# Performance work log

Hardware: AMD Instinct MI355X
Metric: run time of the kernel (lower is better)

The kernel has to match this reference:

```python
import jax, jax.numpy as jnp
import numpy as np

NUM_HEADS = 16


def _local_attn(q, k, v, bias, nq, nk):
    """Blocked local attention, faithful to rearrange_to_dense_trunk semantics.
    q,k,v: [B,H,N,D]; bias: [B,Hb,N,N] (Hb broadcasts against H).
    Trunk i (queries [i*nq,(i+1)*nq)) attends keys at original indices
    [i*nq - pad_left, i*nq - pad_left + nk); out-of-range keys/values/bias are
    zero-padded (the module pads with zeros, no -inf key masking).
    Assumes N % nq == 0 (q_pad_length == 0, so the query mask loop is a no-op).
    """
    B, H, N, D = q.shape
    T = N // nq                      # n_trunks
    pad_left = (nk - nq) // 2
    Lp = (T - 1) * nq + nk           # padded key length so every window is full
    pad_right = Lp - pad_left - N
    k_p = jnp.pad(k, ((0, 0), (0, 0), (pad_left, pad_right), (0, 0)))
    v_p = jnp.pad(v, ((0, 0), (0, 0), (pad_left, pad_right), (0, 0)))
    b_p = jnp.pad(bias, ((0, 0), (0, 0), (0, 0), (pad_left, pad_right)))
    # window gather indices: [T, nk]
    kidx = jnp.arange(T)[:, None] * nq + jnp.arange(nk)[None, :]
    k_t = k_p[:, :, kidx, :]         # [B,H,T,nk,D]
    v_t = v_p[:, :, kidx, :]         # [B,H,T,nk,D]
    Bb, Hb = bias.shape[0], bias.shape[1]
    b_r = b_p.reshape(Bb, Hb, T, nq, Lp)
    b_t = jnp.take_along_axis(b_r, kidx[None, None, :, None, :], axis=-1)  # [Bb,Hb,T,nq,nk]
    q_t = q.reshape(B, H, T, nq, D)
    scores = jnp.einsum('bhtqd,bhtkd->bhtqk', q_t, k_t) + b_t
    w = jax.nn.softmax(scores, axis=-1)
    o = jnp.einsum('bhtqk,bhtkd->bhtqd', w, v_t)
    return o.reshape(B, H, N, D)


def setup_inputs() -> dict:
    key = jax.random.key(0)
    ks = jax.random.split(key, 8)
    B, N, C = 1, 4096, 256
    H, D = NUM_HEADS, 64
    HD = H * D
    q_x = jax.random.normal(ks[0], (B, N, C), dtype=jnp.float32)
    kv_x = jax.random.normal(ks[1], (B, N, C), dtype=jnp.float32)
    attn_bias = jax.random.normal(ks[2], (B, 1, N, N), dtype=jnp.float32) * 0.1
    Wq = jax.random.normal(ks[3], (C, HD), dtype=jnp.float32) / np.sqrt(C).astype(np.float32)
    Wk = jax.random.normal(ks[4], (C, HD), dtype=jnp.float32) / np.sqrt(C).astype(np.float32)
    Wv = jax.random.normal(ks[5], (C, HD), dtype=jnp.float32) / np.sqrt(C).astype(np.float32)
    Wg = jax.random.normal(ks[6], (C, HD), dtype=jnp.float32) / np.sqrt(C).astype(np.float32)
    Wo = jax.random.normal(ks[7], (HD, C), dtype=jnp.float32) / np.sqrt(HD).astype(np.float32)
    return {"q_x": q_x, "kv_x": kv_x, "attn_bias": attn_bias,
            "Wq": Wq, "Wk": Wk, "Wv": Wv, "Wg": Wg, "Wo": Wo,
            "n_queries": 64, "n_keys": 256}


def reference(q_x, kv_x, attn_bias, Wq, Wk, Wv, Wg, Wo, n_queries, n_keys):
    B, N, C = q_x.shape
    H = NUM_HEADS
    D = Wq.shape[-1] // H
    def split_heads(x):
        return x.reshape(B, N, H, D).transpose(0, 2, 1, 3)  # [B,H,N,D]
    q = split_heads(q_x @ Wq) / jnp.sqrt(jnp.float32(D))
    k = split_heads(kv_x @ Wk)
    v = split_heads(kv_x @ Wv)
    o = _local_attn(q, k, v, attn_bias, n_queries, n_keys)
    o = o.transpose(0, 2, 1, 3).reshape(B, N, H * D)
    g = jax.nn.sigmoid(q_x @ Wg)  # gating head
    return (o * g) @ Wo
```

## Files before the change

### kernel.cpp

```cpp
#include <hip/hip_runtime.h>

#define N_ 4096
#define C_ 256
#define H_ 16
#define D_ 64
#define HD_ 1024

typedef __attribute__((ext_vector_type(8))) __bf16 bf16x8;
typedef __attribute__((ext_vector_type(4))) __bf16 bf16x4;
typedef __attribute__((ext_vector_type(8))) _Float16 f16x8;
typedef __attribute__((ext_vector_type(4))) _Float16 f16x4;
typedef __attribute__((ext_vector_type(4))) float f32x4;

__device__ __forceinline__ void gload16(const void* g, void* l) {
    __builtin_amdgcn_global_load_lds(
        (const __attribute__((address_space(1))) unsigned int*)g,
        (__attribute__((address_space(3))) unsigned int*)l, 16, 0, 0);
}

struct bf2 { __bf16 h, l; };
__device__ __forceinline__ bf2 split_bf16(float v) {
    bf2 r;
    r.h = (__bf16)v;
    r.l = (__bf16)(v - (float)r.h);
    return r;
}

__global__ __launch_bounds__(256) void convert_kernel(
    const float* __restrict__ q_x, const float* __restrict__ kv_x,
    const float* __restrict__ Wq, const float* __restrict__ Wk,
    const float* __restrict__ Wv, const float* __restrict__ Wg,
    const float* __restrict__ Wo,
    _Float16* __restrict__ Xf, _Float16* __restrict__ WTf,
    __bf16* __restrict__ WoTh, __bf16* __restrict__ WoTl)
{
    __shared__ float ts[64][65];
    const int b = blockIdx.x;
    const int tid = threadIdx.x;

    if (b < 512) {
        const int seg = b >> 8;
        const float* src = seg ? kv_x : q_x;
        _Float16* df = Xf + (size_t)seg * 1048576;
        const int base = (b & 255) * 4096 + tid * 16;
#pragma unroll
        for (int q = 0; q < 4; ++q) {
            float4 v = *(const float4*)&src[base + q * 4];
            f16x4 fv;
            fv[0] = (_Float16)v.x; fv[1] = (_Float16)v.y;
            fv[2] = (_Float16)v.z; fv[3] = (_Float16)v.w;
            *(f16x4*)&df[base + q * 4] = fv;
        }
        return;
    }

    if (b < 768) {
        const int widx = (b - 512) >> 6;
        const int tile = (b - 512) & 63;
        const float* src = (widx == 0) ? Wq : (widx == 1) ? Wk : (widx == 2) ? Wv : Wg;
        _Float16* df = WTf + (size_t)widx * 262144;
        const int r0 = (tile >> 4) * 64;
        const int c0 = (tile & 15) * 64;
        {
            const int r = tid >> 2;
            const int cch = (tid & 3) * 16;
#pragma unroll
            for (int q = 0; q < 4; ++q) {
                float4 v = *(const float4*)&src[(size_t)(r0 + r) * 1024 + c0 + cch + q * 4];
                ts[r][cch + q * 4 + 0] = v.x;
                ts[r][cch + q * 4 + 1] = v.y;
                ts[r][cch + q * 4 + 2] = v.z;
                ts[r][cch + q * 4 + 3] = v.w;
            }
        }
        __syncthreads();
        {
            const int c = tid >> 2;
            const int rch = (tid & 3) * 16;
#pragma unroll
            for (int q = 0; q < 4; ++q) {
                f16x4 fv;
#pragma unroll
                for (int j = 0; j < 4; ++j)
                    fv[j] = (_Float16)ts[rch + q * 4 + j][c];
                *(f16x4*)&df[(size_t)(c0 + c) * 256 + r0 + rch + q * 4] = fv;
            }
        }
        return;
    }

    {
        const int tile = b - 768;
        const int r0 = (tile >> 2) * 64;
        const int c0 = (tile & 3) * 64;
        {
            const int r = tid >> 2;
            const int cch = (tid & 3) * 16;
#pragma unroll
            for (int q = 0; q < 4; ++q) {
                float4 v = *(const float4*)&Wo[(size_t)(r0 + r) * 256 + c0 + cch + q * 4];
                ts[r][cch + q * 4 + 0] = v.x;
                ts[r][cch + q * 4 + 1] = v.y;
                ts[r][cch + q * 4 + 2] = v.z;
                ts[r][cch + q * 4 + 3] = v.w;
            }
        }
        __syncthreads();
        {
            const int c = tid >> 2;
            const int rch = (tid & 3) * 16;
#pragma unroll
            for (int q = 0; q < 4; ++q) {
                bf16x4 hv, lv;
#pragma unroll
                for (int j = 0; j < 4; ++j) {
                    bf2 s = split_bf16(ts[rch + q * 4 + j][c]);
                    hv[j] = s.h; lv[j] = s.l;
                }
                *(bf16x4*)&WoTh[(size_t)(c0 + c) * 1024 + r0 + rch + q * 4] = hv;
                *(bf16x4*)&WoTl[(size_t)(c0 + c) * 1024 + r0 + rch + q * 4] = lv;
            }
        }
    }
}

__global__ __launch_bounds__(256) void proj_mfma(
    const _Float16* __restrict__ Xf, const _Float16* __restrict__ WTf,
    _Float16* __restrict__ qh, _Float16* __restrict__ kh,
    _Float16* __restrict__ vh, _Float16* __restrict__ gh)
{
    __shared__ __align__(16) char psmem[34816];
    _Float16* As = (_Float16*)psmem;
    _Float16* Bs = (_Float16*)(psmem + 16384);

    const int lb  = blockIdx.x;
    const int xcd = lb & 7;
    const int gr  = (lb >> 6) * 8 + xcd;
    const int g   = gr >> 5;
    const int m0  = (gr & 31) * 128;
    const int c0  = ((lb >> 3) & 7) * 128;

    const _Float16* A = Xf + ((g == 1 || g == 2) ? 1048576 : 0);
    const _Float16* B = WTf + (size_t)g * 262144;

    const int tid  = threadIdx.x;
    const int wave = tid >> 6;
    const int lane = tid & 63;
    const int wr   = wave >> 1;
    const int wc   = wave & 1;
    const int frow = lane & 15;
    const int grp  = lane >> 4;

    f32x4 acc[4][4];
#pragma unroll
    for (int i = 0; i < 4; ++i)
#pragma unroll
        for (int j = 0; j < 4; ++j) acc[i][j] = (f32x4){0.f, 0.f, 0.f, 0.f};

    const int srow = tid >> 3;
    const int sch  = tid & 7;

    for (int kt = 0; kt < 256; kt += 64) {
        __syncthreads();
#pragma unroll
        for (int p = 0; p < 4; ++p) {
            const int row = p * 32 + srow;
            const int koff = kt + ((sch ^ (row & 7)) << 3);
            gload16(A + (size_t)(m0 + row) * 256 + koff, (char*)As + p * 4096 + tid * 16);
            gload16(B + (size_t)(c0 + row) * 256 + koff, (char*)Bs + p * 4096 + tid * 16);
        }
        __syncthreads();

#pragma unroll
        for (int ks = 0; ks < 2; ++ks) {
            f16x8 af[4], bf[4];
#pragma unroll
            for (int f = 0; f < 4; ++f) {
                const int ra = wr * 64 + f * 16 + frow;
                const int rb = wc * 64 + f * 16 + frow;
                af[f] = *(const f16x8*)((char*)As + ra * 128 + (((ks * 4 + grp) ^ (ra & 7)) << 4));
                bf[f] = *(const f16x8*)((char*)Bs + rb * 128 + (((ks * 4 + grp) ^ (rb & 7)) << 4));
            }
#pragma unroll
            for (int i = 0; i < 4; ++i)
#pragma unroll
                for (int j = 0; j < 4; ++j)
                    acc[i][j] = __builtin_amdgcn_mfma_f32_16x16x32_f16(af[i], bf[j], acc[i][j], 0, 0, 0);
        }
    }

    __syncthreads();
    _Float16* Epi = (_Float16*)psmem;
    {
        const float scale = (g == 0) ? 0.125f : 1.f;
#pragma unroll
        for (int i = 0; i < 4; ++i)
#pragma unroll
            for (int j = 0; j < 4; ++j) {
                const int rr = wr * 64 + i * 16 + grp * 4;
                const int cc = wc * 64 + j * 16 + frow;
#pragma unroll
                for (int v = 0; v < 4; ++v) {
                    float x = acc[i][j][v];
                    x = (g == 3) ? 1.f / (1.f + __expf(-x)) : x * scale;
                    Epi[(rr + v) * 136 + cc] = (_Float16)x;
                }
            }
    }
    __syncthreads();
    {
        const int ch   = tid & 15;
        const int head = ch >> 3;
        const int e8   = (ch & 7) * 8;
#pragma unroll
        for (int p = 0; p < 8; ++p) {
            const int r = p * 16 + (tid >> 4);
            const f16x8 val = *(const f16x8*)&Epi[r * 136 + head * 64 + e8];
            if (g == 3) {
                *(f16x8*)&gh[(size_t)(m0 + r) * HD_ + c0 + head * 64 + e8] = val;
            } else {
                _Float16* dst = (g == 0) ? qh : (g == 1) ? kh : vh;
                const int hh = (c0 >> 6) + head;
                *(f16x8*)&dst[((size_t)hh * N_ + m0 + r) * D_ + e8] = val;
            }
        }
    }
}

__global__ __launch_bounds__(256) void attn_mfma(
    const _Float16* __restrict__ qh, const _Float16* __restrict__ kh,
    const _Float16* __restrict__ vh, const float* __restrict__ bias,
    const _Float16* __restrict__ gh,
    __bf16* __restrict__ o_hi, __bf16* __restrict__ o_lo)
{
    __shared__ __align__(16) char smem[59392];
    _Float16* Qs = (_Float16*)smem;
    char* Ks = smem + 8192;
    _Float16* Vs = (_Float16*)(smem + 8192);
    _Float16* Ps = (_Float16*)(smem + 25600);
    float* Oe = (float*)(smem + 25600);

    const int lb  = blockIdx.x;
    const int xcd = lb & 7;
    const int j_  = lb >> 3;
    const int h   = j_ >> 3;
    const int t   = xcd * 8 + (j_ & 7);
    const int tid = threadIdx.x;
    const int lane = tid & 63;
    const int wv = tid >> 6;
    const int frow = lane & 15;
    const int grp = lane >> 4;
    const int kbase = t * 64 - 96;

    const char* qbase = (const char*)qh + (size_t)(h * N_ + t * 64) * 128;
    const char* kbase_p = (const char*)kh + (size_t)h * N_ * 128;

#pragma unroll
    for (int q = 0; q < 2; ++q) {
        const int lin = q * 4096 + tid * 16;
        const int row = lin >> 7;
        const int ch = (lin >> 4) & 7;
        gload16(qbase + row * 128 + ((ch ^ (row & 7)) << 4), (char*)Qs + lin);
    }

    f32x4 sacc[16];

#pragma unroll
    for (int p = 0; p < 2; ++p) {
#pragma unroll
        for (int q = 0; q < 4; ++q) {
            const int lin = q * 4096 + tid * 16;
            const int row = lin >> 7;
            const int ch = (lin >> 4) & 7;
            const int kg = kbase + p * 128 + row;
            if ((unsigned)kg < (unsigned)N_) {
                gload16(kbase_p + (size_t)kg * 128 + ((ch ^ (row & 7)) << 4), Ks + lin);
            } else {
                *(float4*)(Ks + lin) = make_float4(0.f, 0.f, 0.f, 0.f);
            }
        }
        {
            const int rowg = t * 64 + wv * 16 + grp * 4;
#pragma unroll
            for (int j = 0; j < 8; ++j) {
                const int colg = kbase + p * 128 + j * 16 + frow;
                const bool ok = (unsigned)colg < (unsigned)N_;
#pragma unroll
                for (int v = 0; v < 4; ++v)
                    sacc[p * 8 + j][v] = ok ? bias[(size_t)(rowg + v) * N_ + colg] : 0.f;
            }
        }
        __syncthreads();
        const int rq = wv * 16 + frow;
#pragma unroll
        for (int ks = 0; ks < 2; ++ks) {
            const f16x8 aq = *(const f16x8*)((char*)Qs + rq * 128 + (((ks * 4 + grp) ^ (rq & 7)) << 4));
#pragma unroll
            for (int j = 0; j < 8; ++j) {
                const int rk = j * 16 + frow;
                const f16x8 bk = *(const f16x8*)(Ks + rk * 128 + (((ks * 4 + grp) ^ (rk & 7)) << 4));
                sacc[p * 8 + j] = __builtin_amdgcn_mfma_f32_16x16x32_f16(aq, bk, sacc[p * 8 + j], 0, 0, 0);
            }
        }
        __syncthreads();
    }

    float inv[4];
#pragma unroll
    for (int v = 0; v < 4; ++v) {
        float m = sacc[0][v];
#pragma unroll
        for (int f = 1; f < 16; ++f) m = fmaxf(m, sacc[f][v]);
        m = fmaxf(m, __shfl_xor(m, 1));
        m = fmaxf(m, __shfl_xor(m, 2));
        m = fmaxf(m, __shfl_xor(m, 4));
        m = fmaxf(m, __shfl_xor(m, 8));
        float l = 0.f;
#pragma unroll
        for (int f = 0; f < 16; ++f) {
            float e = __expf(sacc[f][v] - m);
            sacc[f][v] = e;
            l += e;
        }
        l += __shfl_xor(l, 1);
        l += __shfl_xor(l, 2);
        l += __shfl_xor(l, 4);
        l += __shfl_xor(l, 8);
        inv[v] = 1.f / l;
    }

    {
        const int rb = wv * 16 + grp * 4;
#pragma unroll
        for (int f = 0; f < 16; ++f) {
            const int col = (f >> 3) * 128 + (f & 7) * 16 + frow;
#pragma unroll
            for (int v = 0; v < 4; ++v)
                Ps[(rb + v) * 264 + col] = (_Float16)sacc[f][v];
        }
    }

    f32x4 oacc[4];
#pragma unroll
    for (int jd = 0; jd < 4; ++jd) oacc[jd] = (f32x4){0.f, 0.f, 0.f, 0.f};

#pragma unroll
    for (int c = 0; c < 2; ++c) {
        {
            const int sl = tid >> 1;
            const int d0 = (tid & 1) * 32;
            const int kg = kbase + c * 128 + sl;
            f16x8 vv[4];
            if ((unsigned)kg < (unsigned)N_) {
                const f16x8* vp = (const f16x8*)(vh + ((size_t)h * N_ + kg) * D_ + d0);
#pragma unroll
                for (int q = 0; q < 4; ++q) vv[q] = vp[q];
            } else {
#pragma unroll
                for (int q = 0; q < 4; ++q)
#pragma unroll
                    for (int e = 0; e < 8; ++e) vv[q][e] = (_Float16)0.f;
            }
#pragma unroll
            for (int q = 0; q < 4; ++q)
#pragma unroll
                for (int e = 0; e < 8; ++e)
                    Vs[(d0 + q * 8 + e) * 136 + sl] = vv[q][e];
        }
        __syncthreads();
        const int rp = wv * 16 + frow;
#pragma unroll
        for (int ks = 0; ks < 4; ++ks) {
            const f16x8 ap = *(const f16x8*)((char*)Ps + rp * 528 + c * 256 + ks * 64 + grp * 16);
#pragma unroll
            for (int jd = 0; jd < 4; ++jd) {
                const f16x8 bv = *(const f16x8*)((char*)Vs + (jd * 16 + frow) * 272 + ks * 64 + grp * 16);
                oacc[jd] = __builtin_amdgcn_mfma_f32_16x16x32_f16(ap, bv, oacc[jd], 0, 0, 0);
            }
        }
        __syncthreads();
    }

#pragma unroll
    for (int jd = 0; jd < 4; ++jd) {
        const int dcol = jd * 16 + frow;
#pragma unroll
        for (int v = 0; v < 4; ++v) {
            const int rn = wv * 16 + grp * 4 + v;
            Oe[rn * 68 + dcol] = oacc[jd][v] * inv[v];
        }
    }
    __syncthreads();
    {
        const int r   = tid >> 2;
        const int seg = tid & 3;
        const int n   = t * 64 + r;
        const int cg0 = h * 64 + seg * 16;
        const float* orow = &Oe[r * 68 + seg * 16];
        f32x4 o0 = *(const f32x4*)&orow[0];
        f32x4 o1 = *(const f32x4*)&orow[4];
        f32x4 o2 = *(const f32x4*)&orow[8];
        f32x4 o3 = *(const f32x4*)&orow[12];
        const f16x8 g0 = *(const f16x8*)&gh[(size_t)n * HD_ + cg0];
        const f16x8 g1 = *(const f16x8*)&gh[(size_t)n * HD_ + cg0 + 8];
        float vals[16];
#pragma unroll
        for (int e = 0; e < 4; ++e) {
            vals[e]      = o0[e] * (float)g0[e];
            vals[4 + e]  = o1[e] * (float)g0[4 + e];
            vals[8 + e]  = o2[e] * (float)g1[e];
            vals[12 + e] = o3[e] * (float)g1[4 + e];
        }
        bf16x8 hi0, hi1, lo0, lo1;
#pragma unroll
        for (int e = 0; e < 8; ++e) {
            bf2 s0 = split_bf16(vals[e]);
            bf2 s1 = split_bf16(vals[8 + e]);
            hi0[e] = s0.h; lo0[e] = s0.l;
            hi1[e] = s1.h; lo1[e] = s1.l;
        }
        *(bf16x8*)&o_hi[(size_t)n * HD_ + cg0]     = hi0;
        *(bf16x8*)&o_hi[(size_t)n * HD_ + cg0 + 8] = hi1;
        *(bf16x8*)&o_lo[(size_t)n * HD_ + cg0]     = lo0;
        *(bf16x8*)&o_lo[(size_t)n * HD_ + cg0 + 8] = lo1;
    }
}

__global__ __launch_bounds__(256) void out_mfma(
    const __bf16* __restrict__ o_hi, const __bf16* __restrict__ o_lo,
    const __bf16* __restrict__ WoTh, const __bf16* __restrict__ WoTl,
    float* __restrict__ out)
{
    __shared__ __align__(16) __bf16 smem[4 * 4096];
    __bf16* As_h = smem;
    __bf16* As_l = smem + 4096;
    __bf16* Bs_h = smem + 8192;
    __bf16* Bs_l = smem + 12288;

    const int lb  = blockIdx.x;
    const int xcd = lb & 7;
    const int idx = lb >> 3;
    const int rowg = (idx >> 2) * 8 + xcd;
    const int m0  = rowg * 64;
    const int c0  = (idx & 3) * 64;

    const int tid  = threadIdx.x;
    const int wave = tid >> 6;
    const int lane = tid & 63;
    const int wr   = wave >> 1;
    const int wc   = wave & 1;
    const int frow = lane & 15;
    const int grp  = lane >> 4;

    f32x4 acc[2][2];
#pragma unroll
    for (int i = 0; i < 2; ++i)
#pragma unroll
        for (int j = 0; j < 2; ++j) acc[i][j] = (f32x4){0.f, 0.f, 0.f, 0.f};

    for (int kt = 0; kt < 1024; kt += 64) {
        __syncthreads();
#pragma unroll
        for (int p = 0; p < 2; ++p) {
            const int lin = p * 4096 + tid * 16;
            const int row = lin >> 7;
            const int ch  = (lin >> 4) & 7;
            const int koff = kt + ((ch ^ (row & 7)) << 3);
            gload16(o_hi + (size_t)(m0 + row) * HD_ + koff, (char*)As_h + lin);
            gload16(o_lo + (size_t)(m0 + row) * HD_ + koff, (char*)As_l + lin);
            gload16(WoTh + (size_t)(c0 + row) * HD_ + koff, (char*)Bs_h + lin);
            gload16(WoTl + (size_t)(c0 + row) * HD_ + koff, (char*)Bs_l + lin);
        }
        __syncthreads();

#pragma unroll
        for (int ks = 0; ks < 2; ++ks) {
            bf16x8 afh[2], afl[2], bfh[2], bfl[2];
#pragma unroll
            for (int f = 0; f < 2; ++f) {
                const int ra = wr * 32 + f * 16 + frow;
                const int rb = wc * 32 + f * 16 + frow;
                const int ca = ((ks * 4 + grp) ^ (ra & 7)) << 4;
                const int cb = ((ks * 4 + grp) ^ (rb & 7)) << 4;
                afh[f] = *(const bf16x8*)((char*)As_h + ra * 128 + ca);
                afl[f] = *(const bf16x8*)((char*)As_l + ra * 128 + ca);
                bfh[f] = *(const bf16x8*)((char*)Bs_h + rb * 128 + cb);
                bfl[f] = *(const bf16x8*)((char*)Bs_l + rb * 128 + cb);
            }
#pragma unroll
            for (int i = 0; i < 2; ++i)
#pragma unroll
                for (int j = 0; j < 2; ++j) {
                    acc[i][j] = __builtin_amdgcn_mfma_f32_16x16x32_bf16(afh[i], bfh[j], acc[i][j], 0, 0, 0);
                    acc[i][j] = __builtin_amdgcn_mfma_f32_16x16x32_bf16(afl[i], bfh[j], acc[i][j], 0, 0, 0);
                    acc[i][j] = __builtin_amdgcn_mfma_f32_16x16x32_bf16(afh[i], bfl[j], acc[i][j], 0, 0, 0);
                }
        }
    }

    const int rbase = grp * 4;
#pragma unroll
    for (int i = 0; i < 2; ++i)
#pragma unroll
        for (int j = 0; j < 2; ++j) {
            const int c = c0 + wc * 32 + j * 16 + frow;
#pragma unroll
            for (int v = 0; v < 4; ++v) {
                const int n = m0 + wr * 32 + i * 16 + rbase + v;
                out[(size_t)n * C_ + c] = acc[i][j][v];
            }
        }
}

extern "C" void kernel_launch(void* const* d_in, const int* in_sizes, int n_in,
                              void* d_out, int out_size, void* d_ws, size_t ws_size,
                              hipStream_t stream)
{
    const float* q_x  = (const float*)d_in[0];
    const float* kv_x = (const float*)d_in[1];
    const float* bias = (const float*)d_in[2];
    const float* Wq   = (const float*)d_in[3];
    const float* Wk   = (const float*)d_in[4];
    const float* Wv   = (const float*)d_in[5];
    const float* Wg   = (const float*)d_in[6];
    const float* Wo   = (const float*)d_in[7];
    float* out = (float*)d_out;

    char* ws = (char*)d_ws;
    const size_t MB = 1048576;
    _Float16* qh  = (_Float16*)(ws);
    _Float16* kh  = (_Float16*)(ws + 8  * MB);
    _Float16* vh  = (_Float16*)(ws + 16 * MB);
    _Float16* gh  = (_Float16*)(ws + 24 * MB);
    __bf16* o_hi  = (__bf16*)(ws + 32 * MB);
    __bf16* o_lo  = (__bf16*)(ws + 40 * MB);
    _Float16* Xf  = (_Float16*)(ws + 48 * MB);
    _Float16* WTf = (_Float16*)(ws + 52 * MB);
    __bf16* WoTh  = (__bf16*)(ws + 54 * MB);
    __bf16* WoTl  = (__bf16*)(ws + 54 * MB + 524288);

    convert_kernel<<<832, 256, 0, stream>>>(q_x, kv_x, Wq, Wk, Wv, Wg, Wo,
                                            Xf, WTf, WoTh, WoTl);
    proj_mfma<<<1024, 256, 0, stream>>>(Xf, WTf, qh, kh, vh, gh);
    attn_mfma<<<1024, 256, 0, stream>>>(qh, kh, vh, bias, gh, o_hi, o_lo);
    out_mfma<<<256, 256, 0, stream>>>(o_hi, o_lo, WoTh, WoTl, out);
}
```

Measured before the change: 173.4 us.

## Use single fp16 output projection and shrink attention LDS footprint

Replaces the split-bf16 (hi/lo, 3-MFMA) output projection with a single fp16 operand path, so the attention output and Wo are each stored once in fp16 and out_mfma issues one MFMA per tile. The attention kernel now writes the P tile per key chunk into a smaller buffer that aliases Q/K space, cutting LDS from 59KB to 34KB, and adds a launch bound hint of 4 blocks per CU to raise occupancy. Together these reduce memory traffic, MFMA count and LDS pressure. The cost is lower precision in the final GEMM, since the fp16 rounding of gated outputs and weights replaces the near-fp32 split emulation, plus possible register pressure from the occupancy hint.

```diff
diff --git a/kernel.cpp b/kernel.cpp
--- a/kernel.cpp
+++ b/kernel.cpp
@@ -7,7 +7,6 @@
 #define HD_ 1024
 
 typedef __attribute__((ext_vector_type(8))) __bf16 bf16x8;
-typedef __attribute__((ext_vector_type(4))) __bf16 bf16x4;
 typedef __attribute__((ext_vector_type(8))) _Float16 f16x8;
 typedef __attribute__((ext_vector_type(4))) _Float16 f16x4;
 typedef __attribute__((ext_vector_type(4))) float f32x4;
@@ -16,14 +15,6 @@
     __builtin_amdgcn_global_load_lds(
         (const __attribute__((address_space(1))) unsigned int*)g,
         (__attribute__((address_space(3))) unsigned int*)l, 16, 0, 0);
-}
-
-struct bf2 { __bf16 h, l; };
-__device__ __forceinline__ bf2 split_bf16(float v) {
-    bf2 r;
-    r.h = (__bf16)v;
-    r.l = (__bf16)(v - (float)r.h);
-    return r;
 }
 
 __global__ __launch_bounds__(256) void convert_kernel(
@@ -32,7 +23,7 @@
     const float* __restrict__ Wv, const float* __restrict__ Wg,
     const float* __restrict__ Wo,
     _Float16* __restrict__ Xf, _Float16* __restrict__ WTf,
-    __bf16* __restrict__ WoTh, __bf16* __restrict__ WoTl)
+    _Float16* __restrict__ WoTf)
 {
     __shared__ float ts[64][65];
     const int b = blockIdx.x;
@@ -54,72 +45,47 @@
         return;
     }
 
+    const float* src;
+    _Float16* df;
+    int srcC, dstC, r0, c0;
     if (b < 768) {
         const int widx = (b - 512) >> 6;
         const int tile = (b - 512) & 63;
-        const float* src = (widx == 0) ? Wq : (widx == 1) ? Wk : (widx == 2) ? Wv : Wg;
-        _Float16* df = WTf + (size_t)widx * 262144;
-        const int r0 = (tile >> 4) * 64;
-        const int c0 = (tile & 15) * 64;
-        {
-            const int r = tid >> 2;
-            const int cch = (tid & 3) * 16;
-#pragma unroll
-            for (int q = 0; q < 4; ++q) {
-                float4 v = *(const float4*)&src[(size_t)(r0 + r) * 1024 + c0 + cch + q * 4];
-                ts[r][cch + q * 4 + 0] = v.x;
-                ts[r][cch + q * 4 + 1] = v.y;
-                ts[r][cch + q * 4 + 2] = v.z;
-                ts[r][cch + q * 4 + 3] = v.w;
-            }
-        }
-        __syncthreads();
-        {
-            const int c = tid >> 2;
-            const int rch = (tid & 3) * 16;
-#pragma unroll
-            for (int q = 0; q < 4; ++q) {
-                f16x4 fv;
-#pragma unroll
-                for (int j = 0; j < 4; ++j)
-                    fv[j] = (_Float16)ts[rch + q * 4 + j][c];
-                *(f16x4*)&df[(size_t)(c0 + c) * 256 + r0 + rch + q * 4] = fv;
-            }
-        }
-        return;
-    }
-
+        src = (widx == 0) ? Wq : (widx == 1) ? Wk : (widx == 2) ? Wv : Wg;
+        df = WTf + (size_t)widx * 262144;
+        srcC = 1024; dstC = 256;
+        r0 = (tile >> 4) * 64;
+        c0 = (tile & 15) * 64;
+    } else {
+        const int tile = b - 768;
+        src = Wo; df = WoTf;
+        srcC = 256; dstC = 1024;
+        r0 = (tile >> 2) * 64;
+        c0 = (tile & 3) * 64;
+    }
     {
-        const int tile = b - 768;
-        const int r0 = (tile >> 2) * 64;
-        const int c0 = (tile & 3) * 64;
-        {
-            const int r = tid >> 2;
-            const int cch = (tid & 3) * 16;
-#pragma unroll
-            for (int q = 0; q < 4; ++q) {
-                float4 v = *(const float4*)&Wo[(size_t)(r0 + r) * 256 + c0 + cch + q * 4];
-                ts[r][cch + q * 4 + 0] = v.x;
-                ts[r][cch + q * 4 + 1] = v.y;
-                ts[r][cch + q * 4 + 2] = v.z;
-                ts[r][cch + q * 4 + 3] = v.w;
-            }
-        }
-        __syncthreads();
-        {
-            const int c = tid >> 2;
-            const int rch = (tid & 3) * 16;
-#pragma unroll
-            for (int q = 0; q < 4; ++q) {
-                bf16x4 hv, lv;
-#pragma unroll
-                for (int j = 0; j < 4; ++j) {
-                    bf2 s = split_bf16(ts[rch + q * 4 + j][c]);
-                    hv[j] = s.h; lv[j] = s.l;
-                }
-                *(bf16x4*)&WoTh[(size_t)(c0 + c) * 1024 + r0 + rch + q * 4] = hv;
-                *(bf16x4*)&WoTl[(size_t)(c0 + c) * 1024 + r0 + rch + q * 4] = lv;
-            }
+        const int r = tid >> 2;
+        const int cch = (tid & 3) * 16;
+#pragma unroll
+        for (int q = 0; q < 4; ++q) {
+            float4 v = *(const float4*)&src[(size_t)(r0 + r) * srcC + c0 + cch + q * 4];
+            ts[r][cch + q * 4 + 0] = v.x;
+            ts[r][cch + q * 4 + 1] = v.y;
+            ts[r][cch + q * 4 + 2] = v.z;
+            ts[r][cch + q * 4 + 3] = v.w;
+        }
+    }
+    __syncthreads();
+    {
+        const int c = tid >> 2;
+        const int rch = (tid & 3) * 16;
+#pragma unroll
+        for (int q = 0; q < 4; ++q) {
+            f16x4 fv;
+#pragma unroll
+            for (int j = 0; j < 4; ++j)
+                fv[j] = (_Float16)ts[rch + q * 4 + j][c];
+            *(f16x4*)&df[(size_t)(c0 + c) * dstC + r0 + rch + q * 4] = fv;
         }
     }
 }
@@ -227,18 +193,17 @@
     }
 }
 
-__global__ __launch_bounds__(256) void attn_mfma(
+__global__ __launch_bounds__(256, 4) void attn_mfma(
     const _Float16* __restrict__ qh, const _Float16* __restrict__ kh,
     const _Float16* __restrict__ vh, const float* __restrict__ bias,
-    const _Float16* __restrict__ gh,
-    __bf16* __restrict__ o_hi, __bf16* __restrict__ o_lo)
+    const _Float16* __restrict__ gh, _Float16* __restrict__ of)
 {
-    __shared__ __align__(16) char smem[59392];
+    __shared__ __align__(16) char smem[34816];
     _Float16* Qs = (_Float16*)smem;
     char* Ks = smem + 8192;
-    _Float16* Vs = (_Float16*)(smem + 8192);
-    _Float16* Ps = (_Float16*)(smem + 25600);
-    float* Oe = (float*)(smem + 25600);
+    _Float16* Ps = (_Float16*)smem;
+    _Float16* Vs = (_Float16*)(smem + 17408);
+    float* Oe = (float*)smem;
 
     const int lb  = blockIdx.x;
     const int xcd = lb & 7;
@@ -329,17 +294,6 @@
         inv[v] = 1.f / l;
     }
 
-    {
-        const int rb = wv * 16 + grp * 4;
-#pragma unroll
-        for (int f = 0; f < 16; ++f) {
-            const int col = (f >> 3) * 128 + (f & 7) * 16 + frow;
-#pragma unroll
-            for (int v = 0; v < 4; ++v)
-                Ps[(rb + v) * 264 + col] = (_Float16)sacc[f][v];
-        }
-    }
-
     f32x4 oacc[4];
 #pragma unroll
     for (int jd = 0; jd < 4; ++jd) oacc[jd] = (f32x4){0.f, 0.f, 0.f, 0.f};
@@ -367,11 +321,21 @@
                 for (int e = 0; e < 8; ++e)
                     Vs[(d0 + q * 8 + e) * 136 + sl] = vv[q][e];
         }
+        {
+            const int rb = wv * 16 + grp * 4;
+#pragma unroll
+            for (int j = 0; j < 8; ++j) {
+                const int col = j * 16 + frow;
+#pragma unroll
+                for (int v = 0; v < 4; ++v)
+                    Ps[(rb + v) * 136 + col] = (_Float16)sacc[c * 8 + j][v];
+            }
+        }
         __syncthreads();
         const int rp = wv * 16 + frow;
 #pragma unroll
         for (int ks = 0; ks < 4; ++ks) {
-            const f16x8 ap = *(const f16x8*)((char*)Ps + rp * 528 + c * 256 + ks * 64 + grp * 16);
+            const f16x8 ap = *(const f16x8*)((char*)Ps + rp * 272 + ks * 64 + grp * 16);
 #pragma unroll
             for (int jd = 0; jd < 4; ++jd) {
                 const f16x8 bv = *(const f16x8*)((char*)Vs + (jd * 16 + frow) * 272 + ks * 64 + grp * 16);
@@ -403,39 +367,26 @@
         f32x4 o3 = *(const f32x4*)&orow[12];
         const f16x8 g0 = *(const f16x8*)&gh[(size_t)n * HD_ + cg0];
         const f16x8 g1 = *(const f16x8*)&gh[(size_t)n * HD_ + cg0 + 8];
-        float vals[16];
+        f16x8 r0, r1;
 #pragma unroll
         for (int e = 0; e < 4; ++e) {
-            vals[e]      = o0[e] * (float)g0[e];
-            vals[4 + e]  = o1[e] * (float)g0[4 + e];
-            vals[8 + e]  = o2[e] * (float)g1[e];
-            vals[12 + e] = o3[e] * (float)g1[4 + e];
-        }
-        bf16x8 hi0, hi1, lo0, lo1;
-#pragma unroll
-        for (int e = 0; e < 8; ++e) {
-            bf2 s0 = split_bf16(vals[e]);
-            bf2 s1 = split_bf16(vals[8 + e]);
-            hi0[e] = s0.h; lo0[e] = s0.l;
-            hi1[e] = s1.h; lo1[e] = s1.l;
-        }
-        *(bf16x8*)&o_hi[(size_t)n * HD_ + cg0]     = hi0;
-        *(bf16x8*)&o_hi[(size_t)n * HD_ + cg0 + 8] = hi1;
-        *(bf16x8*)&o_lo[(size_t)n * HD_ + cg0]     = lo0;
-        *(bf16x8*)&o_lo[(size_t)n * HD_ + cg0 + 8] = lo1;
+            r0[e]     = (_Float16)(o0[e] * (float)g0[e]);
+            r0[4 + e] = (_Float16)(o1[e] * (float)g0[4 + e]);
+            r1[e]     = (_Float16)(o2[e] * (float)g1[e]);
+            r1[4 + e] = (_Float16)(o3[e] * (float)g1[4 + e]);
+        }
+        *(f16x8*)&of[(size_t)n * HD_ + cg0]     = r0;
+        *(f16x8*)&of[(size_t)n * HD_ + cg0 + 8] = r1;
     }
 }
 
 __global__ __launch_bounds__(256) void out_mfma(
-    const __bf16* __restrict__ o_hi, const __bf16* __restrict__ o_lo,
-    const __bf16* __restrict__ WoTh, const __bf16* __restrict__ WoTl,
+    const _Float16* __restrict__ of, const _Float16* __restrict__ WoTf,
     float* __restrict__ out)
 {
-    __shared__ __align__(16) __bf16 smem[4 * 4096];
-    __bf16* As_h = smem;
-    __bf16* As_l = smem + 4096;
-    __bf16* Bs_h = smem + 8192;
-    __bf16* Bs_l = smem + 12288;
+    __shared__ __align__(16) _Float16 smem[2 * 4096];
+    _Float16* As = smem;
+    _Float16* Bs = smem + 4096;
 
     const int lb  = blockIdx.x;
     const int xcd = lb & 7;
@@ -466,35 +417,26 @@
             const int row = lin >> 7;
             const int ch  = (lin >> 4) & 7;
             const int koff = kt + ((ch ^ (row & 7)) << 3);
-            gload16(o_hi + (size_t)(m0 + row) * HD_ + koff, (char*)As_h + lin);
-            gload16(o_lo + (size_t)(m0 + row) * HD_ + koff, (char*)As_l + lin);
-            gload16(WoTh + (size_t)(c0 + row) * HD_ + koff, (char*)Bs_h + lin);
-            gload16(WoTl + (size_t)(c0 + row) * HD_ + koff, (char*)Bs_l + lin);
+            gload16(of   + (size_t)(m0 + row) * HD_ + koff, (char*)As + lin);
+            gload16(WoTf + (size_t)(c0 + row) * HD_ + koff, (char*)Bs + lin);
         }
         __syncthreads();
 
 #pragma unroll
         for (int ks = 0; ks < 2; ++ks) {
-            bf16x8 afh[2], afl[2], bfh[2], bfl[2];
+            f16x8 af[2], bf[2];
 #pragma unroll
             for (int f = 0; f < 2; ++f) {
                 const int ra = wr * 32 + f * 16 + frow;
                 const int rb = wc * 32 + f * 16 + frow;
-                const int ca = ((ks * 4 + grp) ^ (ra & 7)) << 4;
-                const int cb = ((ks * 4 + grp) ^ (rb & 7)) << 4;
-                afh[f] = *(const bf16x8*)((char*)As_h + ra * 128 + ca);
-                afl[f] = *(const bf16x8*)((char*)As_l + ra * 128 + ca);
-                bfh[f] = *(const bf16x8*)((char*)Bs_h + rb * 128 + cb);
-                bfl[f] = *(const bf16x8*)((char*)Bs_l + rb * 128 + cb);
+                af[f] = *(const f16x8*)((char*)As + ra * 128 + (((ks * 4 + grp) ^ (ra & 7)) << 4));
+                bf[f] = *(const f16x8*)((char*)Bs + rb * 128 + (((ks * 4 + grp) ^ (rb & 7)) << 4));
             }
 #pragma unroll
             for (int i = 0; i < 2; ++i)
 #pragma unroll
-                for (int j = 0; j < 2; ++j) {
-                    acc[i][j] = __builtin_amdgcn_mfma_f32_16x16x32_bf16(afh[i], bfh[j], acc[i][j], 0, 0, 0);
-                    acc[i][j] = __builtin_amdgcn_mfma_f32_16x16x32_bf16(afl[i], bfh[j], acc[i][j], 0, 0, 0);
-                    acc[i][j] = __builtin_amdgcn_mfma_f32_16x16x32_bf16(afh[i], bfl[j], acc[i][j], 0, 0, 0);
-                }
+                for (int j = 0; j < 2; ++j)
+                    acc[i][j] = __builtin_amdgcn_mfma_f32_16x16x32_f16(af[i], bf[j], acc[i][j], 0, 0, 0);
         }
     }
 
@@ -528,20 +470,18 @@
 
     char* ws = (char*)d_ws;
     const size_t MB = 1048576;
-    _Float16* qh  = (_Float16*)(ws);
-    _Float16* kh  = (_Float16*)(ws + 8  * MB);
-    _Float16* vh  = (_Float16*)(ws + 16 * MB);
-    _Float16* gh  = (_Float16*)(ws + 24 * MB);
-    __bf16* o_hi  = (__bf16*)(ws + 32 * MB);
-    __bf16* o_lo  = (__bf16*)(ws + 40 * MB);
-    _Float16* Xf  = (_Float16*)(ws + 48 * MB);
-    _Float16* WTf = (_Float16*)(ws + 52 * MB);
-    __bf16* WoTh  = (__bf16*)(ws + 54 * MB);
-    __bf16* WoTl  = (__bf16*)(ws + 54 * MB + 524288);
+    _Float16* qh   = (_Float16*)(ws);
+    _Float16* kh   = (_Float16*)(ws + 8  * MB);
+    _Float16* vh   = (_Float16*)(ws + 16 * MB);
+    _Float16* gh   = (_Float16*)(ws + 24 * MB);
+    _Float16* of   = (_Float16*)(ws + 32 * MB);
+    _Float16* Xf   = (_Float16*)(ws + 40 * MB);
+    _Float16* WTf  = (_Float16*)(ws + 44 * MB);
+    _Float16* WoTf = (_Float16*)(ws + 46 * MB);
 
     convert_kernel<<<832, 256, 0, stream>>>(q_x, kv_x, Wq, Wk, Wv, Wg, Wo,
-                                            Xf, WTf, WoTh, WoTl);
+                                            Xf, WTf, WoTf);
     proj_mfma<<<1024, 256, 0, stream>>>(Xf, WTf, qh, kh, vh, gh);
-    attn_mfma<<<1024, 256, 0, stream>>>(qh, kh, vh, bias, gh, o_hi, o_lo);
-    out_mfma<<<256, 256, 0, stream>>>(o_hi, o_lo, WoTh, WoTl, out);
-}
+    attn_mfma<<<1024, 256, 0, stream>>>(qh, kh, vh, bias, gh, of);
+    out_mfma<<<256, 256, 0, stream>>>(of, WoTf, out);
+}
```

Measured after the change: 163.7 us. 1.06x faster.
